# Optimization experiments

Measured on AMD Instinct MI355X. Metric: run time of the kernel, lower is better.

## Reference

```python
import jax, jax.numpy as jnp
import numpy as np

KP, KD = 25, 3          # keypoints_num, keypoint_dim
FEAT = KP * KD          # 75
H = 1024                # hidden_size
NOISE_VALUE = 0.0
HT_LIMIT = 1.0


def lstm_cell(x, h, c, Wih, Whh, bih, bhh):
    # PyTorch LSTMCell gate order: i, f, g, o
    gates = x @ Wih.T + bih + h @ Whh.T + bhh  # [B, 4H]
    i, f, g, o = jnp.split(gates, 4, axis=-1)
    c = jax.nn.sigmoid(f) * c + jax.nn.sigmoid(i) * jnp.tanh(g)
    h = jax.nn.sigmoid(o) * jnp.tanh(c)
    return h, c


def run_lstm(seq, Wih, Whh, bih, bhh):
    # seq: [T, B, F]; single-layer LSTM, zero init state. Returns final (h, c).
    B = seq.shape[1]
    h0 = jnp.zeros((B, Whh.shape[1]), seq.dtype)
    def step(carry, x):
        h, c = lstm_cell(x, carry[0], carry[1], Wih, Whh, bih, bhh)
        return (h, c), None
    (h, c), _ = jax.lax.scan(step, (h0, h0), seq)
    return h, c


def setup_inputs() -> dict:
    key = jax.random.key(0)
    ks = jax.random.split(key, 20)
    s = 0.02
    inp = {
        'observed_pose': jax.random.normal(ks[0], (1024, 50, FEAT), jnp.float32),
        'future_pose': jax.random.normal(ks[1], (1024, 25, FEAT), jnp.float32),
        'observed_noise': jax.random.randint(ks[2], (1024, 50, KP), 0, 2, jnp.int32),
        # pose encoder LSTM params
        'pe_Wih': jax.random.normal(ks[3], (4 * H, FEAT), jnp.float32) * s,
        'pe_Whh': jax.random.normal(ks[4], (4 * H, H), jnp.float32) * s,
        'pe_bih': jax.random.normal(ks[5], (4 * H,), jnp.float32) * s,
        'pe_bhh': jax.random.normal(ks[6], (4 * H,), jnp.float32) * s,
        # vel encoder LSTM params
        've_Wih': jax.random.normal(ks[7], (4 * H, FEAT), jnp.float32) * s,
        've_Whh': jax.random.normal(ks[8], (4 * H, H), jnp.float32) * s,
        've_bih': jax.random.normal(ks[9], (4 * H,), jnp.float32) * s,
        've_bhh': jax.random.normal(ks[10], (4 * H,), jnp.float32) * s,
        # decoder LSTMCell params
        'dec_Wih': jax.random.normal(ks[11], (4 * H, FEAT), jnp.float32) * s,
        'dec_Whh': jax.random.normal(ks[12], (4 * H, H), jnp.float32) * s,
        'dec_bih': jax.random.normal(ks[13], (4 * H,), jnp.float32) * s,
        'dec_bhh': jax.random.normal(ks[14], (4 * H,), jnp.float32) * s,
        # output projection
        'fc_W': jax.random.normal(ks[15], (FEAT, H), jnp.float32) * s,
        'fc_b': jax.random.normal(ks[16], (FEAT,), jnp.float32) * s,
    }
    return inp


def reference(observed_pose, future_pose, observed_noise,
              pe_Wih, pe_Whh, pe_bih, pe_bhh,
              ve_Wih, ve_Whh, ve_bih, ve_bhh,
              dec_Wih, dec_Whh, dec_bih, dec_bhh,
              fc_W, fc_b):
    pose = observed_pose                              # [B, T, FEAT]
    vel = pose[:, 1:, :] - pose[:, :-1, :]            # [B, T-1, FEAT]
    bs, fn, feat = vel.shape
    noise = observed_noise[:, 1:, :]                  # [B, T-1, KP]
    mask = (noise == 1)[..., None]                    # [B, T-1, KP, 1]
    vel = jnp.where(mask, jnp.float32(NOISE_VALUE),
                    vel.reshape(bs, fn, KP, KD)).reshape(bs, fn, feat)

    h_vel, c_vel = run_lstm(vel.transpose(1, 0, 2), ve_Wih, ve_Whh, ve_bih, ve_bhh)
    h_pose, c_pose = run_lstm(pose.transpose(1, 0, 2), pe_Wih, pe_Whh, pe_bih, pe_bhh)

    h = h_pose + h_vel
    c = c_pose + c_vel
    out0 = vel[:, -1, :]                              # decoder seed input

    def dec_step(carry, _):
        h, c, out = carry
        x = jax.lax.stop_gradient(out)                # .detach() in the original
        h, c = lstm_cell(x, h, c, dec_Wih, dec_Whh, dec_bih, dec_bhh)
        out = jnp.clip(h @ fc_W.T + fc_b, -HT_LIMIT, HT_LIMIT)  # Hardtanh
        return (h, c, out), out

    _, comp_vel = jax.lax.scan(dec_step, (h, c, out0), None, length=fn)
    comp_vel = comp_vel.transpose(1, 0, 2)            # [B, T-1, FEAT]

    # comp_pose[0] = pose[0]; comp_pose[i+1] = comp_pose[i] + comp_vel[i]
    comp_pose = jnp.concatenate(
        [pose[:, :1], pose[:, :1] + jnp.cumsum(comp_vel, axis=1)], axis=1)

    return future_pose, comp_pose, comp_vel
```

## Files before the change

### kernel.cpp

```cpp
#include <hip/hip_runtime.h>

typedef unsigned short ushort_t;
typedef __attribute__((ext_vector_type(8))) short bf16x8;
typedef __attribute__((ext_vector_type(4))) float f32x4;

#define B_    1024
#define H_    1024
#define FEAT_ 75
#define KP_   1120
#define NK_   35
#define OFF_CP 1920000UL
#define OFF_CV 5760000UL

__device__ __forceinline__ float bf2f(ushort_t u) {
    unsigned x = ((unsigned)u) << 16;
    float f; __builtin_memcpy(&f, &x, 4); return f;
}
__device__ __forceinline__ ushort_t f2bf(float f) {
    unsigned x; __builtin_memcpy(&x, &f, 4);
    x += 0x7fffu + ((x >> 16) & 1u);
    return (ushort_t)(x >> 16);
}
__device__ __forceinline__ float sigm(float x) { return 1.f / (1.f + __expf(-x)); }

__device__ __forceinline__ void gload16(const void* g, void* l) {
    __builtin_amdgcn_global_load_lds(
        (const __attribute__((address_space(1))) void*)g,
        (__attribute__((address_space(3))) void*)l, 16, 0, 0);
}

struct StepArgs {
    const ushort_t* Ain[2];
    ushort_t*       Aout[2];
    const ushort_t* W[2];
    const float*    bias[2];
    float*          c[2];
    const ushort_t* xnext[2];
    int             xstride[2];
};

__global__ __launch_bounds__(256)
void lstm_step_kernel(StepArgs sa)
{
    __shared__ __align__(16) char lds[2 * 20480];

    const int p = blockIdx.z;
    const ushort_t* __restrict__ Ain  = sa.Ain[p];
    ushort_t*       __restrict__ Aout = sa.Aout[p];
    const ushort_t* __restrict__ Wt   = sa.W[p];
    const float*    __restrict__ bias = sa.bias[p];
    float*          __restrict__ cst  = sa.c[p];
    const ushort_t* xnext = sa.xnext[p];
    const int xstride = sa.xstride[p];

    const int tid  = threadIdx.x;
    const int w    = tid >> 6;
    const int l    = tid & 63;
    const int ct   = blockIdx.x;
    const int rt   = blockIdx.y;
    const int j0   = ct * 64;
    const int row0 = rt * 64;

    if (ct == 0 && xnext) {
        for (int idx = tid; idx < 64 * 96; idx += 256) {
            const int r  = idx / 96;
            const int xi = idx - r * 96;
            const int grow = row0 + r;
            ushort_t v = (xi < FEAT_) ? xnext[(size_t)grow * xstride + xi] : (ushort_t)0;
            Aout[(size_t)grow * KP_ + 1024 + xi] = v;
        }
    }

    const int lc4  = l & 3;
    const int lr4  = l >> 2;
    const int csrc = lc4 ^ (lr4 & 3);

    const ushort_t* agsrc = Ain + (size_t)(row0 + w * 16 + lr4) * KP_ + csrc * 8;
    char* aldst = lds + (w * 16) * 64;

    const ushort_t* bgsrc[4];
    char* bldst[4];
    #pragma unroll
    for (int i = 0; i < 4; ++i) {
        const int wcol = w * 1024 + j0 + i * 16 + lr4;
        bgsrc[i] = Wt + (size_t)wcol * KP_ + csrc * 8;
        bldst[i] = lds + 4096 + (w * 64 + i * 16) * 64;
    }

    const int chsw = (((l >> 4) ^ (l & 3)) << 4);
    int aoff[4], boff[4];
    #pragma unroll
    for (int m = 0; m < 4; ++m) aoff[m] = (m * 16 + (l & 15)) * 64 + chsw;
    #pragma unroll
    for (int g = 0; g < 4; ++g) boff[g] = 4096 + (g * 64 + w * 16 + (l & 15)) * 64 + chsw;

    f32x4 acc[4][4];
    #pragma unroll
    for (int m = 0; m < 4; ++m)
        #pragma unroll
        for (int g = 0; g < 4; ++g)
            acc[m][g] = (f32x4){0.f, 0.f, 0.f, 0.f};

    {
        const size_t k0 = 0;
        gload16(agsrc + k0, aldst);
        #pragma unroll
        for (int i = 0; i < 4; ++i) gload16(bgsrc[i] + k0, bldst[i]);
    }
    __syncthreads();

    int bi = 0;
    for (int kt = 0; kt < NK_; ++kt) {
        if (kt + 1 < NK_) {
            const size_t k0 = (size_t)(kt + 1) * 32;
            const int nb = (bi ^ 1) * 20480;
            gload16(agsrc + k0, aldst + nb);
            #pragma unroll
            for (int i = 0; i < 4; ++i) gload16(bgsrc[i] + k0, bldst[i] + nb);
        }
        const char* bp = lds + bi * 20480;
        bf16x8 a[4], b[4];
        #pragma unroll
        for (int m = 0; m < 4; ++m) a[m] = *(const bf16x8*)(bp + aoff[m]);
        #pragma unroll
        for (int g = 0; g < 4; ++g) b[g] = *(const bf16x8*)(bp + boff[g]);
        #pragma unroll
        for (int m = 0; m < 4; ++m)
            #pragma unroll
            for (int g = 0; g < 4; ++g)
                acc[m][g] = __builtin_amdgcn_mfma_f32_16x16x32_bf16(a[m], b[g], acc[m][g], 0, 0, 0);
        __syncthreads();
        bi ^= 1;
    }

    const int jw = j0 + w * 16 + (l & 15);
    #pragma unroll
    for (int m = 0; m < 4; ++m) {
        #pragma unroll
        for (int r = 0; r < 4; ++r) {
            const int grow = row0 + m * 16 + ((l >> 4) << 2) + r;
            const float gi = acc[m][0][r] + bias[jw];
            const float gf = acc[m][1][r] + bias[1024 + jw];
            const float gg = acc[m][2][r] + bias[2048 + jw];
            const float go = acc[m][3][r] + bias[3072 + jw];
            const size_t ce = (size_t)grow * H_ + jw;
            const float cn = sigm(gf) * cst[ce] + sigm(gi) * tanhf(gg);
            cst[ce] = cn;
            Aout[(size_t)grow * KP_ + jw] = f2bf(sigm(go) * tanhf(cn));
        }
    }
}

__global__ __launch_bounds__(256)
void pack_kernel(const float* __restrict__ peWih, const float* __restrict__ peWhh,
                 const float* __restrict__ veWih, const float* __restrict__ veWhh,
                 const float* __restrict__ deWih, const float* __restrict__ deWhh,
                 const float* __restrict__ pe_bih, const float* __restrict__ pe_bhh,
                 const float* __restrict__ ve_bih, const float* __restrict__ ve_bhh,
                 const float* __restrict__ de_bih, const float* __restrict__ de_bhh,
                 const float* __restrict__ fcW,
                 ushort_t* __restrict__ Wp, float* __restrict__ biasp,
                 ushort_t* __restrict__ fcWb)
{
    const size_t PER = 4096UL * KP_;
    const size_t NW  = 3UL * PER;
    const size_t NB  = 3UL * 4096;
    const size_t NF  = 75UL * 1024;
    for (size_t idx = (size_t)blockIdx.x * blockDim.x + threadIdx.x;
         idx < NW + NB + NF; idx += (size_t)gridDim.x * blockDim.x) {
        if (idx < NW) {
            const int p   = (int)(idx / PER);
            const size_t rem = idx % PER;
            const int row = (int)(rem / KP_);
            const int k   = (int)(rem % KP_);
            const float* Whh = (p == 0) ? peWhh : (p == 1) ? veWhh : deWhh;
            const float* Wih = (p == 0) ? peWih : (p == 1) ? veWih : deWih;
            float v = 0.f;
            if (k < 1024)      v = Whh[(size_t)row * 1024 + k];
            else if (k < 1099) v = Wih[(size_t)row * 75 + (k - 1024)];
            Wp[idx] = f2bf(v);
        } else if (idx < NW + NB) {
            const size_t i = idx - NW;
            const int p = (int)(i / 4096);
            const int r = (int)(i % 4096);
            const float* bih = (p == 0) ? pe_bih : (p == 1) ? ve_bih : de_bih;
            const float* bhh = (p == 0) ? pe_bhh : (p == 1) ? ve_bhh : de_bhh;
            biasp[i] = bih[r] + bhh[r];
        } else {
            const size_t i = idx - NW - NB;
            fcWb[i] = f2bf(fcW[i]);
        }
    }
}

__global__ __launch_bounds__(256)
void prep_kernel(const float* __restrict__ pose, const float* __restrict__ fut,
                 const int* __restrict__ noise,
                 ushort_t* __restrict__ pose_bf, ushort_t* __restrict__ vel_bf,
                 ushort_t* __restrict__ A_pe0, ushort_t* __restrict__ A_ve0,
                 ushort_t* __restrict__ A_dec0,
                 float* __restrict__ accp, float* __restrict__ out)
{
    const size_t N0 = 1024UL * 50 * 75;
    const size_t N1 = 1024UL * 49 * 75;
    const size_t N2 = 1920000UL;
    const size_t N3 = 76800UL;
    for (size_t idx = (size_t)blockIdx.x * blockDim.x + threadIdx.x;
         idx < N0 + N1 + N2 + N3; idx += (size_t)gridDim.x * blockDim.x) {
        if (idx < N0) {
            pose_bf[idx] = f2bf(pose[idx]);
        } else if (idx < N0 + N1) {
            const size_t i = idx - N0;
            const int f = (int)(i % 75);
            const size_t rem = i / 75;
            const int t = (int)(rem % 49);
            const size_t b = rem / 49;
            float v = pose[(b * 50 + t + 1) * 75 + f] - pose[(b * 50 + t) * 75 + f];
            if (noise[(b * 50 + t + 1) * 25 + f / 3] == 1) v = 0.f;
            const ushort_t vb = f2bf(v);
            vel_bf[i] = vb;
            if (t == 0)  A_ve0[b * KP_ + 1024 + f]  = vb;
            if (t == 48) A_dec0[b * KP_ + 1024 + f] = vb;
        } else if (idx < N0 + N1 + N2) {
            const size_t i = idx - N0 - N1;
            out[i] = fut[i];
        } else {
            const size_t i = idx - N0 - N1 - N2;
            const size_t b = i / 75;
            const int f = (int)(i % 75);
            const float p0 = pose[b * 50 * 75 + f];
            A_pe0[b * KP_ + 1024 + f] = f2bf(p0);
            accp[i] = p0;
            out[OFF_CP + b * 50 * 75 + f] = p0;
        }
    }
}

__global__ __launch_bounds__(256)
void combine_kernel(const ushort_t* __restrict__ hpe, const ushort_t* __restrict__ hve,
                    const float* __restrict__ cpe, const float* __restrict__ cve,
                    ushort_t* __restrict__ Adec0, float* __restrict__ cde)
{
    const int idx = blockIdx.x * blockDim.x + threadIdx.x;
    if (idx >= B_ * H_) return;
    const int b = idx >> 10, j = idx & 1023;
    Adec0[(size_t)b * KP_ + j] = f2bf(bf2f(hpe[(size_t)b * KP_ + j]) + bf2f(hve[(size_t)b * KP_ + j]));
    cde[idx] = cpe[idx] + cve[idx];
}

__global__ __launch_bounds__(128)
void fc_kernel(const ushort_t* __restrict__ Adec,
               ushort_t* __restrict__ Adec_w,
               const ushort_t* __restrict__ fcWb, const float* __restrict__ fcb,
               float* __restrict__ accp, float* __restrict__ out, int t)
{
    __shared__ float hs[1024];
    const int b = blockIdx.x;
    const ushort_t* hrow = Adec + (size_t)b * KP_;
    {
        const int k = threadIdx.x * 8;
        const bf16x8 v = *(const bf16x8*)(hrow + k);
        #pragma unroll
        for (int u = 0; u < 8; ++u) hs[k + u] = bf2f((ushort_t)v[u]);
    }
    __syncthreads();
    const int f = threadIdx.x;
    if (f < FEAT_) {
        const ushort_t* wr = fcWb + (size_t)f * 1024;
        float s = fcb[f];
        for (int k = 0; k < 1024; k += 8) {
            const bf16x8 wv = *(const bf16x8*)(wr + k);
            #pragma unroll
            for (int u = 0; u < 8; ++u) s = fmaf(hs[k + u], bf2f((ushort_t)wv[u]), s);
        }
        s = fminf(fmaxf(s, -1.f), 1.f);
        const float p = accp[b * FEAT_ + f] + s;
        accp[b * FEAT_ + f] = p;
        out[OFF_CV + ((size_t)b * 49 + t) * FEAT_ + f]     = s;
        out[OFF_CP + ((size_t)b * 50 + t + 1) * FEAT_ + f] = p;
        Adec_w[(size_t)b * KP_ + 1024 + f] = f2bf(s);
    }
}

extern "C" void kernel_launch(void* const* d_in, const int* in_sizes, int n_in,
                              void* d_out, int out_size, void* d_ws, size_t ws_size,
                              hipStream_t stream) {
    const float* pose   = (const float*)d_in[0];
    const float* fut    = (const float*)d_in[1];
    const int*   noise  = (const int*)  d_in[2];
    const float* peWih  = (const float*)d_in[3];
    const float* peWhh  = (const float*)d_in[4];
    const float* pe_bih = (const float*)d_in[5];
    const float* pe_bhh = (const float*)d_in[6];
    const float* veWih  = (const float*)d_in[7];
    const float* veWhh  = (const float*)d_in[8];
    const float* ve_bih = (const float*)d_in[9];
    const float* ve_bhh = (const float*)d_in[10];
    const float* deWih  = (const float*)d_in[11];
    const float* deWhh  = (const float*)d_in[12];
    const float* de_bih = (const float*)d_in[13];
    const float* de_bhh = (const float*)d_in[14];
    const float* fcW    = (const float*)d_in[15];
    const float* fcb    = (const float*)d_in[16];
    float* out = (float*)d_out;

    char* base = (char*)d_ws;
    ushort_t* Ape[2]  = {(ushort_t*)(base + 0UL * 2293760), (ushort_t*)(base + 1UL * 2293760)};
    ushort_t* Ave[2]  = {(ushort_t*)(base + 2UL * 2293760), (ushort_t*)(base + 3UL * 2293760)};
    ushort_t* Adec[2] = {(ushort_t*)(base + 4UL * 2293760), (ushort_t*)(base + 5UL * 2293760)};
    float* c_pe = (float*)(base + 13762560);
    float* c_ve = c_pe + 1048576;
    float* c_de = c_ve + 1048576;
    ushort_t* Wp    = (ushort_t*)(base + 26345472);
    float*    biasp = (float*)   (base + 53870592);
    ushort_t* fcWb  = (ushort_t*)(base + 53919744);
    ushort_t* pose_bf = (ushort_t*)(base + 54073344);
    ushort_t* vel_bf  = (ushort_t*)(base + 61753344);
    float*    accp    = (float*)   (base + 69279744);

    hipMemsetAsync(base, 0, 22151168, stream);

    pack_kernel<<<2048, 256, 0, stream>>>(peWih, peWhh, veWih, veWhh, deWih, deWhh,
                                          pe_bih, pe_bhh, ve_bih, ve_bhh, de_bih, de_bhh,
                                          fcW, Wp, biasp, fcWb);
    prep_kernel<<<2048, 256, 0, stream>>>(pose, fut, noise, pose_bf, vel_bf,
                                          Ape[0], Ave[0], Adec[0], accp, out);

    const ushort_t* Wpe = Wp;
    const ushort_t* Wve = Wp + 4587520;
    const ushort_t* Wde = Wp + 9175040;

    for (int t = 0; t < 49; ++t) {
        StepArgs sa;
        sa.Ain[0] = Ape[t & 1];  sa.Aout[0] = Ape[(t + 1) & 1];
        sa.W[0] = Wpe; sa.bias[0] = biasp; sa.c[0] = c_pe;
        sa.xnext[0] = pose_bf + (size_t)(t + 1) * 75; sa.xstride[0] = 3750;
        sa.Ain[1] = Ave[t & 1];  sa.Aout[1] = Ave[(t + 1) & 1];
        sa.W[1] = Wve; sa.bias[1] = biasp + 4096; sa.c[1] = c_ve;
        sa.xnext[1] = (t < 48) ? (vel_bf + (size_t)(t + 1) * 75) : nullptr;
        sa.xstride[1] = 3675;
        lstm_step_kernel<<<dim3(16, 16, 2), 256, 0, stream>>>(sa);
    }
    {
        StepArgs sa;
        sa.Ain[0] = Ape[1]; sa.Aout[0] = Ape[0];
        sa.W[0] = Wpe; sa.bias[0] = biasp; sa.c[0] = c_pe;
        sa.xnext[0] = nullptr; sa.xstride[0] = 3750;
        sa.Ain[1] = sa.Ain[0]; sa.Aout[1] = sa.Aout[0];
        sa.W[1] = sa.W[0]; sa.bias[1] = sa.bias[0]; sa.c[1] = sa.c[0];
        sa.xnext[1] = nullptr; sa.xstride[1] = 3750;
        lstm_step_kernel<<<dim3(16, 16, 1), 256, 0, stream>>>(sa);
    }

    combine_kernel<<<4096, 256, 0, stream>>>(Ape[0], Ave[1], c_pe, c_ve, Adec[0], c_de);

    for (int d = 0; d < 49; ++d) {
        StepArgs sa;
        sa.Ain[0] = Adec[d & 1]; sa.Aout[0] = Adec[(d + 1) & 1];
        sa.W[0] = Wde; sa.bias[0] = biasp + 8192; sa.c[0] = c_de;
        sa.xnext[0] = nullptr; sa.xstride[0] = 0;
        sa.Ain[1] = sa.Ain[0]; sa.Aout[1] = sa.Aout[0];
        sa.W[1] = sa.W[0]; sa.bias[1] = sa.bias[0]; sa.c[1] = sa.c[0];
        sa.xnext[1] = nullptr; sa.xstride[1] = 0;
        lstm_step_kernel<<<dim3(16, 16, 1), 256, 0, stream>>>(sa);
        fc_kernel<<<B_, 128, 0, stream>>>(Adec[(d + 1) & 1], Adec[(d + 1) & 1],
                                          fcWb, fcb, accp, out, d);
    }
}
```

Before: 4.797 ms.

## Remap LSTM step blocks per XCD, tighten k-loop waits, unroll FC reduction

The 3D grid is flattened and remapped so that each of the 8 XCDs gets a contiguous group of weight column tiles. Blocks that share weight slices then share an L2. The k-loop's double-buffered pipeline swaps full __syncthreads for explicit vmcnt waits plus raw barriers, and raises wave priority around the MFMA burst. Bias loads are hoisted out of the epilogue loop, and the FC dot product uses four independent accumulators to shorten the dependency chain. The new waits depend on exact counts of outstanding loads, and the accumulator split changes the FC summation order slightly.

```diff
diff --git a/kernel.cpp b/kernel.cpp
--- a/kernel.cpp
+++ b/kernel.cpp
@@ -44,7 +44,21 @@
 {
     __shared__ __align__(16) char lds[2 * 20480];
 
-    const int p = blockIdx.z;
+    const int flat = blockIdx.x;
+    const int xcd  = flat & 7;
+    const int slot = flat >> 3;
+    int p, ct, rt;
+    if (gridDim.x == 512) {
+        const int cg = (xcd << 2) + (slot >> 4);
+        p  = cg >> 4;
+        ct = cg & 15;
+    } else {
+        const int cg = (xcd << 1) + (slot >> 4);
+        p  = 0;
+        ct = cg;
+    }
+    rt = slot & 15;
+
     const ushort_t* __restrict__ Ain  = sa.Ain[p];
     ushort_t*       __restrict__ Aout = sa.Aout[p];
     const ushort_t* __restrict__ Wt   = sa.W[p];
@@ -56,8 +70,6 @@
     const int tid  = threadIdx.x;
     const int w    = tid >> 6;
     const int l    = tid & 63;
-    const int ct   = blockIdx.x;
-    const int rt   = blockIdx.y;
     const int j0   = ct * 64;
     const int row0 = rt * 64;
 
@@ -101,13 +113,9 @@
         for (int g = 0; g < 4; ++g)
             acc[m][g] = (f32x4){0.f, 0.f, 0.f, 0.f};
 
-    {
-        const size_t k0 = 0;
-        gload16(agsrc + k0, aldst);
-        #pragma unroll
-        for (int i = 0; i < 4; ++i) gload16(bgsrc[i] + k0, bldst[i]);
-    }
-    __syncthreads();
+    gload16(agsrc, aldst);
+    #pragma unroll
+    for (int i = 0; i < 4; ++i) gload16(bgsrc[i], bldst[i]);
 
     int bi = 0;
     for (int kt = 0; kt < NK_; ++kt) {
@@ -117,32 +125,46 @@
             gload16(agsrc + k0, aldst + nb);
             #pragma unroll
             for (int i = 0; i < 4; ++i) gload16(bgsrc[i] + k0, bldst[i] + nb);
-        }
+            asm volatile("s_waitcnt vmcnt(5)" ::: "memory");
+        } else {
+            asm volatile("s_waitcnt vmcnt(0)" ::: "memory");
+        }
+        __builtin_amdgcn_s_barrier();
+        asm volatile("" ::: "memory");
+
         const char* bp = lds + bi * 20480;
         bf16x8 a[4], b[4];
         #pragma unroll
         for (int m = 0; m < 4; ++m) a[m] = *(const bf16x8*)(bp + aoff[m]);
         #pragma unroll
         for (int g = 0; g < 4; ++g) b[g] = *(const bf16x8*)(bp + boff[g]);
+        __builtin_amdgcn_s_setprio(1);
         #pragma unroll
         for (int m = 0; m < 4; ++m)
             #pragma unroll
             for (int g = 0; g < 4; ++g)
                 acc[m][g] = __builtin_amdgcn_mfma_f32_16x16x32_bf16(a[m], b[g], acc[m][g], 0, 0, 0);
-        __syncthreads();
+        __builtin_amdgcn_s_setprio(0);
+
+        asm volatile("" ::: "memory");
+        __builtin_amdgcn_s_barrier();
         bi ^= 1;
     }
 
     const int jw = j0 + w * 16 + (l & 15);
+    const float b_i = bias[jw];
+    const float b_f = bias[1024 + jw];
+    const float b_g = bias[2048 + jw];
+    const float b_o = bias[3072 + jw];
     #pragma unroll
     for (int m = 0; m < 4; ++m) {
         #pragma unroll
         for (int r = 0; r < 4; ++r) {
             const int grow = row0 + m * 16 + ((l >> 4) << 2) + r;
-            const float gi = acc[m][0][r] + bias[jw];
-            const float gf = acc[m][1][r] + bias[1024 + jw];
-            const float gg = acc[m][2][r] + bias[2048 + jw];
-            const float go = acc[m][3][r] + bias[3072 + jw];
+            const float gi = acc[m][0][r] + b_i;
+            const float gf = acc[m][1][r] + b_f;
+            const float gg = acc[m][2][r] + b_g;
+            const float go = acc[m][3][r] + b_o;
             const size_t ce = (size_t)grow * H_ + jw;
             const float cn = sigm(gf) * cst[ce] + sigm(gi) * tanhf(gg);
             cst[ce] = cn;
@@ -267,12 +289,21 @@
     const int f = threadIdx.x;
     if (f < FEAT_) {
         const ushort_t* wr = fcWb + (size_t)f * 1024;
-        float s = fcb[f];
-        for (int k = 0; k < 1024; k += 8) {
-            const bf16x8 wv = *(const bf16x8*)(wr + k);
+        float s0 = fcb[f], s1 = 0.f, s2 = 0.f, s3 = 0.f;
+        for (int k = 0; k < 1024; k += 32) {
+            const bf16x8 w0 = *(const bf16x8*)(wr + k);
+            const bf16x8 w1 = *(const bf16x8*)(wr + k + 8);
+            const bf16x8 w2 = *(const bf16x8*)(wr + k + 16);
+            const bf16x8 w3 = *(const bf16x8*)(wr + k + 24);
             #pragma unroll
-            for (int u = 0; u < 8; ++u) s = fmaf(hs[k + u], bf2f((ushort_t)wv[u]), s);
-        }
+            for (int u = 0; u < 8; ++u) {
+                s0 = fmaf(hs[k + u],      bf2f((ushort_t)w0[u]), s0);
+                s1 = fmaf(hs[k + 8 + u],  bf2f((ushort_t)w1[u]), s1);
+                s2 = fmaf(hs[k + 16 + u], bf2f((ushort_t)w2[u]), s2);
+                s3 = fmaf(hs[k + 24 + u], bf2f((ushort_t)w3[u]), s3);
+            }
+        }
+        float s = (s0 + s1) + (s2 + s3);
         s = fminf(fmaxf(s, -1.f), 1.f);
         const float p = accp[b * FEAT_ + f] + s;
         accp[b * FEAT_ + f] = p;
@@ -339,7 +370,7 @@
         sa.W[1] = Wve; sa.bias[1] = biasp + 4096; sa.c[1] = c_ve;
         sa.xnext[1] = (t < 48) ? (vel_bf + (size_t)(t + 1) * 75) : nullptr;
         sa.xstride[1] = 3675;
-        lstm_step_kernel<<<dim3(16, 16, 2), 256, 0, stream>>>(sa);
+        lstm_step_kernel<<<512, 256, 0, stream>>>(sa);
     }
     {
         StepArgs sa;
@@ -349,7 +380,7 @@
         sa.Ain[1] = sa.Ain[0]; sa.Aout[1] = sa.Aout[0];
         sa.W[1] = sa.W[0]; sa.bias[1] = sa.bias[0]; sa.c[1] = sa.c[0];
         sa.xnext[1] = nullptr; sa.xstride[1] = 3750;
-        lstm_step_kernel<<<dim3(16, 16, 1), 256, 0, stream>>>(sa);
+        lstm_step_kernel<<<256, 256, 0, stream>>>(sa);
     }
 
     combine_kernel<<<4096, 256, 0, stream>>>(Ape[0], Ave[1], c_pe, c_ve, Adec[0], c_de);
@@ -362,7 +393,7 @@
         sa.Ain[1] = sa.Ain[0]; sa.Aout[1] = sa.Aout[0];
         sa.W[1] = sa.W[0]; sa.bias[1] = sa.bias[0]; sa.c[1] = sa.c[0];
         sa.xnext[1] = nullptr; sa.xstride[1] = 0;
-        lstm_step_kernel<<<dim3(16, 16, 1), 256, 0, stream>>>(sa);
+        lstm_step_kernel<<<256, 256, 0, stream>>>(sa);
         fc_kernel<<<B_, 128, 0, stream>>>(Adec[(d + 1) & 1], Adec[(d + 1) & 1],
                                           fcWb, fcb, accp, out, d);
     }
```

Result: faster. 4.061 ms (-15.3%).
